# Optimization experiments

Measured on AMD Instinct MI355X. Metric: run time of the kernel, lower is better.

Reference implementation:

```python
import math
import jax, jax.numpy as jnp
import numpy as np

NEG_INF_FILL = 1e-09  # faithful to the source: masked positions get +1e-09, not -inf

B, H, S, D = 2, 16, 2048, 64


def setup_inputs() -> dict:
    key = jax.random.key(0)
    kq, kk, kv = jax.random.split(key, 3)
    q = jax.random.normal(kq, (B, H, S, D), dtype=jnp.float32)
    k = jax.random.normal(kk, (B, H, S, D), dtype=jnp.float32)
    v = jax.random.normal(kv, (B, H, S, D), dtype=jnp.float32)
    # causal boolean mask, broadcast over heads: [B, 1, S, S]
    causal = jnp.tril(jnp.ones((S, S), dtype=bool))
    attention_mask = jnp.broadcast_to(causal[None, None, :, :], (B, 1, S, S))
    return {"q": q, "k": k, "v": v, "attention_mask": attention_mask}


def reference(q, k, v, attention_mask):
    d_k = q.shape[-1]
    # scores: [B, H, S, S]
    scores = jnp.einsum("bhqd,bhkd->bhqk", q, k) / math.sqrt(d_k)
    scores = jnp.where(attention_mask, scores, NEG_INF_FILL)
    attn = jax.nn.softmax(scores, axis=-1)
    # output: [B, H, S, D]
    return jnp.einsum("bhqk,bhkd->bhqd", attn, v)
```

## Files before the change

### kernel.cpp

```cpp
#include <hip/hip_runtime.h>
#include <hip/hip_bf16.h>


#define SEQ 2048
#define DIM 64
#define KS_STRIDE 72
#define PS_STRIDE 72
#define QSCALE 0.18033688011112042f

typedef _Float16 half_t;
typedef _Float16 half8  __attribute__((ext_vector_type(8)));
typedef _Float16 half4v __attribute__((ext_vector_type(4)));
typedef _Float16 half2v __attribute__((ext_vector_type(2)));
typedef float    float4v __attribute__((ext_vector_type(4)));

__global__ __launch_bounds__(256, 4)
void attn_mfma_kernel(const float* __restrict__ Q,
                      const float* __restrict__ K,
                      const float* __restrict__ V,
                      float* __restrict__ O) {
    __shared__ half_t smem_h[64 * KS_STRIDE + 64 * KS_STRIDE + 4 * 16 * PS_STRIDE];
    half_t* Ks  = smem_h;
    half_t* VTs = smem_h + 64 * KS_STRIDE;
    half_t* Ps  = smem_h + 2 * 64 * KS_STRIDE;

    const int tid = threadIdx.x;
    const int l   = tid & 63;
    const int w   = tid >> 6;
    const int lx  = l & 15;
    const int h   = l >> 4;
    const int bh  = blockIdx.x;
    const int qb  = 31 - (int)blockIdx.y;
    const int qbase = qb * 64;
    const int nkt = qb + 1;
    const int n_tail = SEQ - nkt * 64;

    const float* Qh = Q + (size_t)bh * SEQ * DIM;
    const float* Kh = K + (size_t)bh * SEQ * DIM;
    const float* Vh = V + (size_t)bh * SEQ * DIM;
    float*       Oh = O + (size_t)bh * SEQ * DIM;

    half8 qf[2];
    const int qrow_w = qbase + 16 * w;
    {
        const float* qp = Qh + (size_t)(qrow_w + lx) * DIM;
        #pragma unroll
        for (int s = 0; s < 2; ++s) {
            float4v a = *(const float4v*)(qp + 32 * s + 8 * h);
            float4v b = *(const float4v*)(qp + 32 * s + 8 * h + 4);
            half8 f;
            f[0] = (half_t)(a[0] * QSCALE); f[1] = (half_t)(a[1] * QSCALE);
            f[2] = (half_t)(a[2] * QSCALE); f[3] = (half_t)(a[3] * QSCALE);
            f[4] = (half_t)(b[0] * QSCALE); f[5] = (half_t)(b[1] * QSCALE);
            f[6] = (half_t)(b[2] * QSCALE); f[7] = (half_t)(b[3] * QSCALE);
            qf[s] = f;
        }
    }

    float4v acc[4];
    #pragma unroll
    for (int mt = 0; mt < 4; ++mt) acc[mt] = (float4v){0.f, 0.f, 0.f, 0.f};
    float lp = 0.f;

    const int c  = tid & 15;
    const int r0 = tid >> 4;

    float4v kreg[4], vreg[4];
    auto load_tile = [&](int kt) {
        const float* Kt = Kh + (size_t)kt * 64 * DIM;
        const float* Vt = Vh + (size_t)kt * 64 * DIM;
        #pragma unroll
        for (int u = 0; u < 4; ++u)
            kreg[u] = *(const float4v*)(Kt + (r0 + 16 * u) * DIM + 4 * c);
        #pragma unroll
        for (int u = 0; u < 2; ++u) {
            const float* vp = Vt + (size_t)(2 * (r0 + 16 * u)) * DIM + 4 * c;
            vreg[2 * u]     = *(const float4v*)(vp);
            vreg[2 * u + 1] = *(const float4v*)(vp + DIM);
        }
    };

    load_tile(0);

    for (int kt = 0; kt < nkt; ++kt) {
        __syncthreads();

        #pragma unroll
        for (int u = 0; u < 4; ++u) {
            int kr = r0 + 16 * u;
            half4v hk;
            hk[0] = (half_t)kreg[u][0]; hk[1] = (half_t)kreg[u][1];
            hk[2] = (half_t)kreg[u][2]; hk[3] = (half_t)kreg[u][3];
            *(half4v*)(Ks + kr * KS_STRIDE + 4 * c) = hk;
        }
        #pragma unroll
        for (int u = 0; u < 2; ++u) {
            int kp = r0 + 16 * u;
            #pragma unroll
            for (int i = 0; i < 4; ++i) {
                int ir = (i + c + (c >> 2)) & 3;
                int dr = 4 * c + ir;
                half2v hv;
                hv[0] = (half_t)vreg[2 * u][ir];
                hv[1] = (half_t)vreg[2 * u + 1][ir];
                *(half2v*)(VTs + dr * KS_STRIDE + 2 * kp) = hv;
            }
        }
        __syncthreads();

        if (kt + 1 < nkt) load_tile(kt + 1);

        const int key_base = kt * 64;
        #pragma unroll
        for (int mt = 0; mt < 4; ++mt) {
            half8 ak0 = *(const half8*)(Ks + (16 * mt + lx) * KS_STRIDE + 8 * h);
            half8 ak1 = *(const half8*)(Ks + (16 * mt + lx) * KS_STRIDE + 32 + 8 * h);
            const bool need_mask = (key_base + 16 * mt + 15) > qrow_w;
            float4v ct = (float4v){0.f, 0.f, 0.f, 0.f};
            ct = __builtin_amdgcn_mfma_f32_16x16x32_f16(ak0, qf[0], ct, 0, 0, 0);
            ct = __builtin_amdgcn_mfma_f32_16x16x32_f16(ak1, qf[1], ct, 0, 0, 0);
            float p[4];
            #pragma unroll
            for (int r = 0; r < 4; ++r)
                p[r] = __builtin_amdgcn_exp2f(ct[r]);
            if (need_mask) {
                const int qg = qrow_w + lx;
                const int kb = key_base + 16 * mt + 4 * h;
                #pragma unroll
                for (int r = 0; r < 4; ++r)
                    if (kb + r > qg) p[r] = 1.0f;
            }
            lp += (p[0] + p[1]) + (p[2] + p[3]);
            half4v hp;
            hp[0] = (half_t)p[0]; hp[1] = (half_t)p[1];
            hp[2] = (half_t)p[2]; hp[3] = (half_t)p[3];
            *(half4v*)(Ps + w * (16 * PS_STRIDE) + lx * PS_STRIDE + 16 * mt + 4 * h) = hp;
        }

        half8 pf[2];
        #pragma unroll
        for (int s = 0; s < 2; ++s)
            pf[s] = *(const half8*)(Ps + w * (16 * PS_STRIDE) + lx * PS_STRIDE
                                    + 32 * s + 8 * h);
        #pragma unroll
        for (int mtd = 0; mtd < 4; ++mtd) {
            half8 av0 = *(const half8*)(VTs + (16 * mtd + lx) * KS_STRIDE + 8 * h);
            half8 av1 = *(const half8*)(VTs + (16 * mtd + lx) * KS_STRIDE + 32 + 8 * h);
            float4v ct = acc[mtd];
            ct = __builtin_amdgcn_mfma_f32_16x16x32_f16(av0, pf[0], ct, 0, 0, 0);
            ct = __builtin_amdgcn_mfma_f32_16x16x32_f16(av1, pf[1], ct, 0, 0, 0);
            acc[mtd] = ct;
        }
    }

    float s_l = lp;
    s_l += __shfl_xor(s_l, 16, 64);
    s_l += __shfl_xor(s_l, 32, 64);
    const float linv = 1.0f / (s_l + (float)n_tail);

    float ts0 = 0.f, ts1 = 0.f, ts2 = 0.f, ts3 = 0.f;
    {
        const int tstart = nkt * 64;
        #pragma unroll 4
        for (int k = tstart + r0; k < SEQ; k += 16) {
            float4v x = *(const float4v*)(Vh + (size_t)k * DIM + 4 * c);
            ts0 += x[0]; ts1 += x[1]; ts2 += x[2]; ts3 += x[3];
        }
    }
    __syncthreads();
    float* preS = (float*)smem_h;
    float* vtf  = ((float*)smem_h) + 4160;
    {
        float4v pv = {ts0, ts1, ts2, ts3};
        *(float4v*)(preS + r0 * 68 + 4 * c) = pv;
    }
    __syncthreads();
    if (tid < 64) {
        float s = 0.f;
        #pragma unroll
        for (int p = 0; p < 16; ++p) s += preS[p * 68 + tid];
        vtf[tid] = s;
    }
    __syncthreads();
    float vt_l[4][4];
    #pragma unroll
    for (int mt = 0; mt < 4; ++mt)
        #pragma unroll
        for (int r = 0; r < 4; ++r) vt_l[mt][r] = vtf[16 * mt + 4 * h + r];

    float* Osm = (float*)smem_h;
    #pragma unroll
    for (int mt = 0; mt < 4; ++mt)
        #pragma unroll
        for (int r = 0; r < 4; ++r) {
            float o = (acc[mt][r] + vt_l[mt][r]) * linv;
            Osm[w * (16 * 65) + lx * 65 + 16 * mt + 4 * h + r] = o;
        }
    __syncthreads();
    #pragma unroll
    for (int u = 0; u < 4; ++u) {
        int row = r0 + 16 * u;
        int dc = 4 * c;
        const float* src = Osm + (row >> 4) * (16 * 65) + (row & 15) * 65 + dc;
        float4v ov = {src[0], src[1], src[2], src[3]};
        *(float4v*)(Oh + (size_t)(qbase + row) * DIM + dc) = ov;
    }
}

extern "C" void kernel_launch(void* const* d_in, const int* in_sizes, int n_in,
                              void* d_out, int out_size, void* d_ws, size_t ws_size,
                              hipStream_t stream) {
    const float* q = (const float*)d_in[0];
    const float* k = (const float*)d_in[1];
    const float* v = (const float*)d_in[2];
    float* out = (float*)d_out;
    attn_mfma_kernel<<<dim3(32, 32), 256, 0, stream>>>(q, k, v, out);
}
```

Baseline: 147.3 us.

## Pre-convert K and transposed V to fp16 images in a prep kernel

A new prep kernel converts K to fp16 and writes V transposed in fp16 into workspace, one 64x64 tile per block. The attention kernel then loads ready-made fp16 tiles and copies them straight into LDS, with no per-iteration conversion or transpose scatter, and reads half the bytes for K and V. This adds a second launch and an extra write and read pass over K and V. The old kernel is kept as a fallback for when no workspace is available.

```diff
diff --git a/kernel.cpp b/kernel.cpp
--- a/kernel.cpp
+++ b/kernel.cpp
@@ -1,9 +1,9 @@
 #include <hip/hip_runtime.h>
-#include <hip/hip_bf16.h>
 
 
 #define SEQ 2048
 #define DIM 64
+#define NKT 32
 #define KS_STRIDE 72
 #define PS_STRIDE 72
 #define QSCALE 0.18033688011112042f
@@ -14,12 +14,67 @@
 typedef _Float16 half2v __attribute__((ext_vector_type(2)));
 typedef float    float4v __attribute__((ext_vector_type(4)));
 
+#define KIMG_HALFS ((size_t)4194304)
+#define WS_NEED    ((size_t)16777216)
+
+__global__ __launch_bounds__(256)
+void prep_kernel(const float* __restrict__ K, const float* __restrict__ V,
+                 half_t* __restrict__ Kimg, half_t* __restrict__ VTimg) {
+    __shared__ __align__(16) half_t vt[64 * 72];
+    const int kt = blockIdx.x, bh = blockIdx.y;
+    const int tid = threadIdx.x;
+    const float* Kt = K + ((size_t)bh * SEQ + kt * 64) * DIM;
+    const float* Vt = V + ((size_t)bh * SEQ + kt * 64) * DIM;
+    half_t* Kd = Kimg  + (((size_t)(bh * NKT + kt)) << 12);
+    half_t* Vd = VTimg + (((size_t)(bh * NKT + kt)) << 12);
+
+    {
+        const int row = tid >> 2, q = tid & 3;
+        const float* src = Kt + row * DIM + 16 * q;
+        #pragma unroll
+        for (int cc = 0; cc < 2; ++cc) {
+            float4v a = *(const float4v*)(src + 8 * cc);
+            float4v b = *(const float4v*)(src + 8 * cc + 4);
+            half8 hh;
+            hh[0]=(half_t)a[0]; hh[1]=(half_t)a[1]; hh[2]=(half_t)a[2]; hh[3]=(half_t)a[3];
+            hh[4]=(half_t)b[0]; hh[5]=(half_t)b[1]; hh[6]=(half_t)b[2]; hh[7]=(half_t)b[3];
+            *(half8*)(Kd + row * 64 + 16 * q + 8 * cc) = hh;
+        }
+    }
+    {
+        const int c = tid & 15, r0 = tid >> 4;
+        #pragma unroll
+        for (int u = 0; u < 2; ++u) {
+            const float* vp = Vt + (size_t)(2 * (r0 + 16 * u)) * DIM + 4 * c;
+            float4v x0 = *(const float4v*)(vp);
+            float4v x1 = *(const float4v*)(vp + DIM);
+            #pragma unroll
+            for (int i = 0; i < 4; ++i) {
+                const int d = 4 * c + i;
+                vt[d * 72 + 2 * (r0 + 16 * u)]     = (half_t)x0[i];
+                vt[d * 72 + 2 * (r0 + 16 * u) + 1] = (half_t)x1[i];
+            }
+        }
+    }
+    __syncthreads();
+    {
+        const int d = tid >> 2, g = tid & 3;
+        #pragma unroll
+        for (int cc = 0; cc < 2; ++cc) {
+            const int c0 = 2 * g + cc;
+            half8 hh = *(const half8*)(vt + d * 72 + 8 * c0);
+            *(half8*)(Vd + d * 64 + 8 * c0) = hh;
+        }
+    }
+}
+
 __global__ __launch_bounds__(256, 4)
 void attn_mfma_kernel(const float* __restrict__ Q,
-                      const float* __restrict__ K,
+                      const half_t* __restrict__ Kimg,
+                      const half_t* __restrict__ VTimg,
                       const float* __restrict__ V,
                       float* __restrict__ O) {
-    __shared__ half_t smem_h[64 * KS_STRIDE + 64 * KS_STRIDE + 4 * 16 * PS_STRIDE];
+    __shared__ __align__(16) half_t smem_h[64 * KS_STRIDE + 64 * KS_STRIDE + 4 * 16 * PS_STRIDE];
     half_t* Ks  = smem_h;
     half_t* VTs = smem_h + 64 * KS_STRIDE;
     half_t* Ps  = smem_h + 2 * 64 * KS_STRIDE;
@@ -36,9 +91,10 @@
     const int n_tail = SEQ - nkt * 64;
 
     const float* Qh = Q + (size_t)bh * SEQ * DIM;
-    const float* Kh = K + (size_t)bh * SEQ * DIM;
     const float* Vh = V + (size_t)bh * SEQ * DIM;
     float*       Oh = O + (size_t)bh * SEQ * DIM;
+    const half_t* Kimg_b = Kimg  + (((size_t)(bh * NKT)) << 12);
+    const half_t* Vimg_b = VTimg + (((size_t)(bh * NKT)) << 12);
 
     half8 qf[2];
     const int qrow_w = qbase + 16 * w;
@@ -62,22 +118,17 @@
     for (int mt = 0; mt < 4; ++mt) acc[mt] = (float4v){0.f, 0.f, 0.f, 0.f};
     float lp = 0.f;
 
-    const int c  = tid & 15;
-    const int r0 = tid >> 4;
-
-    float4v kreg[4], vreg[4];
+    const int soff = tid << 3;
+    const int srow = tid >> 3;
+    const int sc8  = (tid & 7) << 3;
+    half8 kh0, kh1, vh0, vh1;
     auto load_tile = [&](int kt) {
-        const float* Kt = Kh + (size_t)kt * 64 * DIM;
-        const float* Vt = Vh + (size_t)kt * 64 * DIM;
-        #pragma unroll
-        for (int u = 0; u < 4; ++u)
-            kreg[u] = *(const float4v*)(Kt + (r0 + 16 * u) * DIM + 4 * c);
-        #pragma unroll
-        for (int u = 0; u < 2; ++u) {
-            const float* vp = Vt + (size_t)(2 * (r0 + 16 * u)) * DIM + 4 * c;
-            vreg[2 * u]     = *(const float4v*)(vp);
-            vreg[2 * u + 1] = *(const float4v*)(vp + DIM);
-        }
+        const half_t* Kt16 = Kimg_b + ((size_t)kt << 12);
+        const half_t* Vt16 = Vimg_b + ((size_t)kt << 12);
+        kh0 = *(const half8*)(Kt16 + soff);
+        kh1 = *(const half8*)(Kt16 + soff + 2048);
+        vh0 = *(const half8*)(Vt16 + soff);
+        vh1 = *(const half8*)(Vt16 + soff + 2048);
     };
 
     load_tile(0);
@@ -85,27 +136,10 @@
     for (int kt = 0; kt < nkt; ++kt) {
         __syncthreads();
 
-        #pragma unroll
-        for (int u = 0; u < 4; ++u) {
-            int kr = r0 + 16 * u;
-            half4v hk;
-            hk[0] = (half_t)kreg[u][0]; hk[1] = (half_t)kreg[u][1];
-            hk[2] = (half_t)kreg[u][2]; hk[3] = (half_t)kreg[u][3];
-            *(half4v*)(Ks + kr * KS_STRIDE + 4 * c) = hk;
-        }
-        #pragma unroll
-        for (int u = 0; u < 2; ++u) {
-            int kp = r0 + 16 * u;
-            #pragma unroll
-            for (int i = 0; i < 4; ++i) {
-                int ir = (i + c + (c >> 2)) & 3;
-                int dr = 4 * c + ir;
-                half2v hv;
-                hv[0] = (half_t)vreg[2 * u][ir];
-                hv[1] = (half_t)vreg[2 * u + 1][ir];
-                *(half2v*)(VTs + dr * KS_STRIDE + 2 * kp) = hv;
-            }
-        }
+        *(half8*)(Ks  + srow * KS_STRIDE + sc8)        = kh0;
+        *(half8*)(Ks  + (srow + 32) * KS_STRIDE + sc8) = kh1;
+        *(half8*)(VTs + srow * KS_STRIDE + sc8)        = vh0;
+        *(half8*)(VTs + (srow + 32) * KS_STRIDE + sc8) = vh1;
         __syncthreads();
 
         if (kt + 1 < nkt) load_tile(kt + 1);
@@ -160,6 +194,203 @@
 
     float ts0 = 0.f, ts1 = 0.f, ts2 = 0.f, ts3 = 0.f;
     {
+        const int c = tid & 15, r0 = tid >> 4;
+        const int tstart = nkt * 64;
+        #pragma unroll 4
+        for (int k = tstart + r0; k < SEQ; k += 16) {
+            float4v x = *(const float4v*)(Vh + (size_t)k * DIM + 4 * c);
+            ts0 += x[0]; ts1 += x[1]; ts2 += x[2]; ts3 += x[3];
+        }
+    }
+    __syncthreads();
+    float* preS = (float*)smem_h;
+    float* vtf  = ((float*)smem_h) + 4160;
+    {
+        const int c = tid & 15, r0 = tid >> 4;
+        float4v pv = {ts0, ts1, ts2, ts3};
+        *(float4v*)(preS + r0 * 68 + 4 * c) = pv;
+    }
+    __syncthreads();
+    if (tid < 64) {
+        float s = 0.f;
+        #pragma unroll
+        for (int p = 0; p < 16; ++p) s += preS[p * 68 + tid];
+        vtf[tid] = s;
+    }
+    __syncthreads();
+    float vt_l[4][4];
+    #pragma unroll
+    for (int mt = 0; mt < 4; ++mt)
+        #pragma unroll
+        for (int r = 0; r < 4; ++r) vt_l[mt][r] = vtf[16 * mt + 4 * h + r];
+
+    float* Osm = (float*)smem_h;
+    #pragma unroll
+    for (int mt = 0; mt < 4; ++mt)
+        #pragma unroll
+        for (int r = 0; r < 4; ++r) {
+            float o = (acc[mt][r] + vt_l[mt][r]) * linv;
+            Osm[w * (16 * 65) + lx * 65 + 16 * mt + 4 * h + r] = o;
+        }
+    __syncthreads();
+    {
+        const int c = tid & 15, r0 = tid >> 4;
+        #pragma unroll
+        for (int u = 0; u < 4; ++u) {
+            const int row = r0 + 16 * u;
+            const int dc = 4 * c;
+            const float* src = Osm + (row >> 4) * (16 * 65) + (row & 15) * 65 + dc;
+            float4v ov = {src[0], src[1], src[2], src[3]};
+            *(float4v*)(Oh + (size_t)(qbase + row) * DIM + dc) = ov;
+        }
+    }
+}
+
+__global__ __launch_bounds__(256, 4)
+void attn_mfma_fallback(const float* __restrict__ Q,
+                        const float* __restrict__ K,
+                        const float* __restrict__ V,
+                        float* __restrict__ O) {
+    __shared__ half_t smem_h[64 * KS_STRIDE + 64 * KS_STRIDE + 4 * 16 * PS_STRIDE];
+    half_t* Ks  = smem_h;
+    half_t* VTs = smem_h + 64 * KS_STRIDE;
+    half_t* Ps  = smem_h + 2 * 64 * KS_STRIDE;
+
+    const int tid = threadIdx.x;
+    const int l   = tid & 63;
+    const int w   = tid >> 6;
+    const int lx  = l & 15;
+    const int h   = l >> 4;
+    const int bh  = blockIdx.x;
+    const int qb  = 31 - (int)blockIdx.y;
+    const int qbase = qb * 64;
+    const int nkt = qb + 1;
+    const int n_tail = SEQ - nkt * 64;
+
+    const float* Qh = Q + (size_t)bh * SEQ * DIM;
+    const float* Kh = K + (size_t)bh * SEQ * DIM;
+    const float* Vh = V + (size_t)bh * SEQ * DIM;
+    float*       Oh = O + (size_t)bh * SEQ * DIM;
+
+    half8 qf[2];
+    const int qrow_w = qbase + 16 * w;
+    {
+        const float* qp = Qh + (size_t)(qrow_w + lx) * DIM;
+        #pragma unroll
+        for (int s = 0; s < 2; ++s) {
+            float4v a = *(const float4v*)(qp + 32 * s + 8 * h);
+            float4v b = *(const float4v*)(qp + 32 * s + 8 * h + 4);
+            half8 f;
+            f[0] = (half_t)(a[0] * QSCALE); f[1] = (half_t)(a[1] * QSCALE);
+            f[2] = (half_t)(a[2] * QSCALE); f[3] = (half_t)(a[3] * QSCALE);
+            f[4] = (half_t)(b[0] * QSCALE); f[5] = (half_t)(b[1] * QSCALE);
+            f[6] = (half_t)(b[2] * QSCALE); f[7] = (half_t)(b[3] * QSCALE);
+            qf[s] = f;
+        }
+    }
+
+    float4v acc[4];
+    #pragma unroll
+    for (int mt = 0; mt < 4; ++mt) acc[mt] = (float4v){0.f, 0.f, 0.f, 0.f};
+    float lp = 0.f;
+
+    const int c  = tid & 15;
+    const int r0 = tid >> 4;
+
+    float4v kreg[4], vreg[4];
+    auto load_tile = [&](int kt) {
+        const float* Kt = Kh + (size_t)kt * 64 * DIM;
+        const float* Vt = Vh + (size_t)kt * 64 * DIM;
+        #pragma unroll
+        for (int u = 0; u < 4; ++u)
+            kreg[u] = *(const float4v*)(Kt + (r0 + 16 * u) * DIM + 4 * c);
+        #pragma unroll
+        for (int u = 0; u < 2; ++u) {
+            const float* vp = Vt + (size_t)(2 * (r0 + 16 * u)) * DIM + 4 * c;
+            vreg[2 * u]     = *(const float4v*)(vp);
+            vreg[2 * u + 1] = *(const float4v*)(vp + DIM);
+        }
+    };
+
+    load_tile(0);
+
+    for (int kt = 0; kt < nkt; ++kt) {
+        __syncthreads();
+        #pragma unroll
+        for (int u = 0; u < 4; ++u) {
+            int kr = r0 + 16 * u;
+            half4v hk;
+            hk[0] = (half_t)kreg[u][0]; hk[1] = (half_t)kreg[u][1];
+            hk[2] = (half_t)kreg[u][2]; hk[3] = (half_t)kreg[u][3];
+            *(half4v*)(Ks + kr * KS_STRIDE + 4 * c) = hk;
+        }
+        #pragma unroll
+        for (int u = 0; u < 2; ++u) {
+            int kp = r0 + 16 * u;
+            #pragma unroll
+            for (int i = 0; i < 4; ++i) {
+                int ir = (i + c + (c >> 2)) & 3;
+                int dr = 4 * c + ir;
+                half2v hv;
+                hv[0] = (half_t)vreg[2 * u][ir];
+                hv[1] = (half_t)vreg[2 * u + 1][ir];
+                *(half2v*)(VTs + dr * KS_STRIDE + 2 * kp) = hv;
+            }
+        }
+        __syncthreads();
+
+        if (kt + 1 < nkt) load_tile(kt + 1);
+
+        const int key_base = kt * 64;
+        #pragma unroll
+        for (int mt = 0; mt < 4; ++mt) {
+            half8 ak0 = *(const half8*)(Ks + (16 * mt + lx) * KS_STRIDE + 8 * h);
+            half8 ak1 = *(const half8*)(Ks + (16 * mt + lx) * KS_STRIDE + 32 + 8 * h);
+            const bool need_mask = (key_base + 16 * mt + 15) > qrow_w;
+            float4v ct = (float4v){0.f, 0.f, 0.f, 0.f};
+            ct = __builtin_amdgcn_mfma_f32_16x16x32_f16(ak0, qf[0], ct, 0, 0, 0);
+            ct = __builtin_amdgcn_mfma_f32_16x16x32_f16(ak1, qf[1], ct, 0, 0, 0);
+            float p[4];
+            #pragma unroll
+            for (int r = 0; r < 4; ++r)
+                p[r] = __builtin_amdgcn_exp2f(ct[r]);
+            if (need_mask) {
+                const int qg = qrow_w + lx;
+                const int kb = key_base + 16 * mt + 4 * h;
+                #pragma unroll
+                for (int r = 0; r < 4; ++r)
+                    if (kb + r > qg) p[r] = 1.0f;
+            }
+            lp += (p[0] + p[1]) + (p[2] + p[3]);
+            half4v hp;
+            hp[0] = (half_t)p[0]; hp[1] = (half_t)p[1];
+            hp[2] = (half_t)p[2]; hp[3] = (half_t)p[3];
+            *(half4v*)(Ps + w * (16 * PS_STRIDE) + lx * PS_STRIDE + 16 * mt + 4 * h) = hp;
+        }
+
+        half8 pf[2];
+        #pragma unroll
+        for (int s = 0; s < 2; ++s)
+            pf[s] = *(const half8*)(Ps + w * (16 * PS_STRIDE) + lx * PS_STRIDE
+                                    + 32 * s + 8 * h);
+        #pragma unroll
+        for (int mtd = 0; mtd < 4; ++mtd) {
+            half8 av0 = *(const half8*)(VTs + (16 * mtd + lx) * KS_STRIDE + 8 * h);
+            half8 av1 = *(const half8*)(VTs + (16 * mtd + lx) * KS_STRIDE + 32 + 8 * h);
+            float4v ct = acc[mtd];
+            ct = __builtin_amdgcn_mfma_f32_16x16x32_f16(av0, pf[0], ct, 0, 0, 0);
+            ct = __builtin_amdgcn_mfma_f32_16x16x32_f16(av1, pf[1], ct, 0, 0, 0);
+            acc[mtd] = ct;
+        }
+    }
+
+    float s_l = lp;
+    s_l += __shfl_xor(s_l, 16, 64);
+    s_l += __shfl_xor(s_l, 32, 64);
+    const float linv = 1.0f / (s_l + (float)n_tail);
+
+    float ts0 = 0.f, ts1 = 0.f, ts2 = 0.f, ts3 = 0.f;
+    {
         const int tstart = nkt * 64;
         #pragma unroll 4
         for (int k = tstart + r0; k < SEQ; k += 16) {
@@ -214,5 +445,13 @@
     const float* k = (const float*)d_in[1];
     const float* v = (const float*)d_in[2];
     float* out = (float*)d_out;
-    attn_mfma_kernel<<<dim3(32, 32), 256, 0, stream>>>(q, k, v, out);
+
+    if (d_ws != nullptr && ws_size >= WS_NEED) {
+        half_t* kimg = (half_t*)d_ws;
+        half_t* vimg = kimg + KIMG_HALFS;
+        prep_kernel<<<dim3(32, 32), 256, 0, stream>>>(k, v, kimg, vimg);
+        attn_mfma_kernel<<<dim3(32, 32), 256, 0, stream>>>(q, kimg, vimg, v, out);
+    } else {
+        attn_mfma_fallback<<<dim3(32, 32), 256, 0, stream>>>(q, k, v, out);
+    }
 }
```

Measured after the change: 144.6 us. Within noise of the previous version (-1.8%).
